# Performance work log

Hardware: AMD Instinct MI355X
Metric: run time of the kernel (lower is better)

Reference implementation:

```python
import jax, jax.numpy as jnp
import numpy as np

N_NODES = 100000
N_EDGES = 1600000
NFEAT, NHID1, NCLASS = 256, 128, 64
NUM_GRAPHS = 64


def gcn_conv(x, edge_index, edge_weight, W, b):
    # PyG GCNConv: linear transform, add self-loops (weight 1), symmetric norm, scatter-add
    n = x.shape[0]
    x = x @ W  # [N, out]
    loop = jnp.arange(n)
    row = jnp.concatenate([edge_index[0], loop])  # source
    col = jnp.concatenate([edge_index[1], loop])  # target
    w = jnp.concatenate([edge_weight, jnp.ones((n,), dtype=x.dtype)])
    deg = jax.ops.segment_sum(w, col, num_segments=n)
    dinv = jnp.where(deg > 0, jax.lax.rsqrt(jnp.maximum(deg, 1e-30)), 0.0)
    norm = dinv[row] * w * dinv[col]  # [E+N]
    out = jax.ops.segment_sum(x[row] * norm[:, None], col, num_segments=n)
    return out + b


def setup_inputs() -> dict:
    key = jax.random.key(0)
    ks = jax.random.split(key, 12)
    x = jax.random.normal(ks[0], (N_NODES, NFEAT), dtype=jnp.float32)
    edge_index = jax.random.randint(ks[1], (2, N_EDGES), 0, N_NODES, dtype=jnp.int64)
    edge_weight = jax.random.uniform(ks[2], (N_EDGES,), dtype=jnp.float32)
    batch = jnp.sort(jax.random.randint(ks[3], (N_NODES,), 0, NUM_GRAPHS, dtype=jnp.int64))
    def glorot(k, shape):
        lim = float(np.sqrt(6.0 / (shape[0] + shape[1])))
        return jax.random.uniform(k, shape, jnp.float32, -lim, lim)
    W1 = glorot(ks[4], (NFEAT, NHID1)); b1 = jnp.zeros((NHID1,), jnp.float32)
    W2 = glorot(ks[5], (NHID1, NCLASS)); b2 = jnp.zeros((NCLASS,), jnp.float32)
    l1w = glorot(ks[6], (NCLASS, 64)); l1b = jnp.zeros((64,), jnp.float32)
    l2w = glorot(ks[7], (64, 2)); l2b = jnp.zeros((2,), jnp.float32)
    return {"x": x, "edge_index": edge_index, "edge_weight": edge_weight, "batch": batch,
            "W1": W1, "b1": b1, "W2": W2, "b2": b2,
            "l1w": l1w, "l1b": l1b, "l2w": l2w, "l2b": l2b}


def reference(x, edge_index, edge_weight, batch, W1, b1, W2, b2, l1w, l1b, l2w, l2b):
    h = jax.nn.relu(gcn_conv(x, edge_index, edge_weight, W1, b1))
    h = jax.nn.relu(gcn_conv(h, edge_index, edge_weight, W2, b2))
    pooled = jax.ops.segment_sum(h, batch, num_segments=NUM_GRAPHS)  # global_add_pool
    h = jax.nn.relu(pooled @ l1w + l1b)
    out = h @ l2w + l2b
    Y_prob = jax.nn.log_softmax(out, axis=1)
    Y_hat = jnp.argmax(Y_prob, axis=1).astype(jnp.float32)
    return (Y_prob, Y_hat, out)
```

## Files before the change

kernel.cpp:

```cpp
#include <hip/hip_runtime.h>
#include <hip/hip_bf16.h>
#include <math.h>

#define N_NODES 100000
#define N_EDGES 1600000
#define NFEAT 256
#define NHID1 128
#define NCLASS 64
#define NUM_GRAPHS 64

#define POOL_CHUNK 64

#define NBUCK 391
#define EPB 8192
#define NBLK_A 196

typedef __attribute__((ext_vector_type(8))) short bf16x8;
typedef __attribute__((ext_vector_type(4))) float f32x4;


__device__ __forceinline__ unsigned short f2bf(float f) {
    unsigned u = __float_as_uint(f);
    u += 0x7fffu + ((u >> 16) & 1u);
    return (unsigned short)(u >> 16);
}
__device__ __forceinline__ unsigned packbf2(float lo, float hi) {
    return (unsigned)f2bf(lo) | ((unsigned)f2bf(hi) << 16);
}
__device__ __forceinline__ float bflo(unsigned p) { return __uint_as_float(p << 16); }
__device__ __forceinline__ float bfhi(unsigned p) { return __uint_as_float(p & 0xffff0000u); }


__global__ __launch_bounds__(256) void hist_kernel(const int* __restrict__ cols,
                                                   int* __restrict__ ghist, int nE) {
    __shared__ int h[NBUCK];
    const int tid = threadIdx.x;
    for (int i = tid; i < NBUCK; i += 256) h[i] = 0;
    __syncthreads();
    long base = (long)blockIdx.x * EPB;
    for (int j = tid; j < EPB; j += 256) {
        long idx = base + j;
        if (idx < nE) atomicAdd(&h[cols[idx] >> 8], 1);
    }
    __syncthreads();
    for (int i = tid; i < NBUCK; i += 256) {
        int v = h[i];
        if (v) atomicAdd(&ghist[i], v);
    }
}


__global__ __launch_bounds__(512) void bucket_scan_kernel(const int* __restrict__ ghist,
                                                          int* __restrict__ gbase,
                                                          int* __restrict__ gcursor) {
    __shared__ int sh[512];
    int t = threadIdx.x;
    int v = (t < NBUCK) ? ghist[t] : 0;
    sh[t] = v;
    __syncthreads();
    for (int off = 1; off < 512; off <<= 1) {
        int add = (t >= off) ? sh[t - off] : 0;
        __syncthreads();
        sh[t] += add;
        __syncthreads();
    }
    if (t < NBUCK) {
        int excl = sh[t] - v;
        gbase[t] = excl;
        gcursor[t] = excl;
    }
}


__global__ __launch_bounds__(256) void scatter_bucket_kernel(const int* __restrict__ rows,
                                                             const int* __restrict__ cols,
                                                             const float* __restrict__ w,
                                                             int* __restrict__ gcursor,
                                                             int2* __restrict__ csc_tmp, int nE) {
    __shared__ int h[NBUCK];
    __shared__ int bb[NBUCK];
    __shared__ unsigned short rk[EPB];
    const int tid = threadIdx.x;
    for (int i = tid; i < NBUCK; i += 256) h[i] = 0;
    __syncthreads();
    long base = (long)blockIdx.x * EPB;
    for (int j = tid; j < EPB; j += 256) {
        long idx = base + j;
        if (idx < nE) rk[j] = (unsigned short)atomicAdd(&h[cols[idx] >> 8], 1);
    }
    __syncthreads();
    for (int i = tid; i < NBUCK; i += 256) {
        int v = h[i];
        if (v) bb[i] = atomicAdd(&gcursor[i], v);
    }
    __syncthreads();
    for (int j = tid; j < EPB; j += 256) {
        long idx = base + j;
        if (idx < nE) {
            int c = cols[idx];
            int b = c >> 8;
            int pos = bb[b] + (int)rk[j];
            csc_tmp[pos] = make_int2((rows[idx] & 0x1FFFF) | ((c & 255) << 17),
                                     __float_as_int(w[idx]));
        }
    }
}


__global__ __launch_bounds__(256) void build_csc_kernel(const int2* __restrict__ csc_tmp,
                                                        const int* __restrict__ gbase,
                                                        const int* __restrict__ ghist,
                                                        int2* __restrict__ edges,
                                                        int* __restrict__ starts,
                                                        int* __restrict__ cnt,
                                                        float* __restrict__ dinv, int n) {
    __shared__ int ncnt[256];
    __shared__ float nws[256];
    __shared__ int sh[256];
    __shared__ int ncur[256];
    const int tid = threadIdx.x;
    const int b = blockIdx.x;
    const int base = gbase[b];
    const int cntb = ghist[b];

    ncnt[tid] = 0;
    nws[tid] = 0.f;
    __syncthreads();

    for (int i = tid; i < cntb; i += 256) {
        int2 rec = csc_tmp[base + i];
        int local = ((unsigned)rec.x) >> 17;
        atomicAdd(&ncnt[local], 1);
        atomicAdd(&nws[local], __int_as_float(rec.y));
    }
    __syncthreads();

    int v = ncnt[tid];
    sh[tid] = v;
    __syncthreads();
    for (int off = 1; off < 256; off <<= 1) {
        int add = (tid >= off) ? sh[tid - off] : 0;
        __syncthreads();
        sh[tid] += add;
        __syncthreads();
    }
    int excl = sh[tid] - v;
    ncur[tid] = excl;

    int node = (b << 8) + tid;
    if (node < n) {
        cnt[node] = v;
        starts[node] = base + excl;
        dinv[node] = rsqrtf(1.0f + nws[tid]);
    }
    __syncthreads();

    for (int i = tid; i < cntb; i += 256) {
        int2 rec = csc_tmp[base + i];
        int local = ((unsigned)rec.x) >> 17;
        int r = rec.x & 0x1FFFF;
        int pos = base + atomicAdd(&ncur[local], 1);
        edges[pos] = make_int2(r, rec.y);
    }
}


__global__ void transpose_bf_kernel(const float* __restrict__ W, unsigned* __restrict__ WT,
                                    int K, int Nn) {
    int idx = blockIdx.x * blockDim.x + threadIdx.x;
    int total = Nn * (K / 2);
    if (idx < total) {
        int n = idx / (K / 2);
        int kp = idx - n * (K / 2);
        WT[idx] = packbf2(W[(2 * kp) * Nn + n], W[(2 * kp + 1) * Nn + n]);
    }
}


template <int NT, int KK, bool ABF16>
__global__ __launch_bounds__(256) void gemm_mfma(const void* __restrict__ Av,
                                                 const unsigned* __restrict__ BT,
                                                 const float* __restrict__ rowscale,
                                                 unsigned short* __restrict__ C,
                                                 int M) {
    constexpr int CT = NT / 16;
    constexpr int KD = KK / 2;
    __shared__ unsigned Al[4][128][4];
    __shared__ unsigned Bl[4][NT][4];
    const int tid = threadIdx.x;
    const int wave = tid >> 6;
    const int lane = tid & 63;
    const int quad = lane >> 4;
    const int l16 = lane & 15;
    const int row0 = blockIdx.x * 128;

    f32x4 acc[2][CT] = {};

    for (int k0 = 0; k0 < KK; k0 += 32) {
        if (ABF16) {
            const unsigned* Ab = (const unsigned*)Av;
            #pragma unroll
            for (int i = 0; i < 2; i++) {
                int idx = tid + i * 256;
                int ar = idx >> 2, aq = idx & 3;
                uint4 v = make_uint4(0, 0, 0, 0);
                if (row0 + ar < M)
                    v = *(const uint4*)(Ab + (long)(row0 + ar) * KD + k0 / 2 + aq * 4);
                *(uint4*)&Al[aq][ar][0] = v;
            }
        } else {
            const float* Af = (const float*)Av;
            int ar = tid >> 1, ah = tid & 1;
            float4 v0 = make_float4(0, 0, 0, 0), v1 = v0, v2 = v0, v3 = v0;
            if (row0 + ar < M) {
                const float* p = Af + (long)(row0 + ar) * KK + k0 + ah * 16;
                v0 = *(const float4*)p;
                v1 = *(const float4*)(p + 4);
                v2 = *(const float4*)(p + 8);
                v3 = *(const float4*)(p + 12);
            }
            uint4 d0 = make_uint4(packbf2(v0.x, v0.y), packbf2(v0.z, v0.w),
                                  packbf2(v1.x, v1.y), packbf2(v1.z, v1.w));
            uint4 d1 = make_uint4(packbf2(v2.x, v2.y), packbf2(v2.z, v2.w),
                                  packbf2(v3.x, v3.y), packbf2(v3.z, v3.w));
            *(uint4*)&Al[ah * 2 + 0][ar][0] = d0;
            *(uint4*)&Al[ah * 2 + 1][ar][0] = d1;
        }
        #pragma unroll
        for (int i = 0; i < NT / 64; i++) {
            int idx = tid + i * 256;
            int br = idx >> 2, bq = idx & 3;
            *(uint4*)&Bl[bq][br][0] = *(const uint4*)(BT + (long)br * KD + k0 / 2 + bq * 4);
        }
        __syncthreads();

        bf16x8 af[2];
        #pragma unroll
        for (int rt = 0; rt < 2; rt++)
            af[rt] = *(const bf16x8*)&Al[quad][wave * 32 + rt * 16 + l16][0];
        #pragma unroll
        for (int ct = 0; ct < CT; ct++) {
            bf16x8 bfr = *(const bf16x8*)&Bl[quad][ct * 16 + l16][0];
            acc[0][ct] = __builtin_amdgcn_mfma_f32_16x16x32_bf16(af[0], bfr, acc[0][ct], 0, 0, 0);
            acc[1][ct] = __builtin_amdgcn_mfma_f32_16x16x32_bf16(af[1], bfr, acc[1][ct], 0, 0, 0);
        }
        __syncthreads();
    }

    #pragma unroll
    for (int rt = 0; rt < 2; rt++) {
        #pragma unroll
        for (int reg = 0; reg < 4; reg++) {
            int row = row0 + wave * 32 + rt * 16 + quad * 4 + reg;
            if (row < M) {
                float sc = rowscale[row];
                unsigned short* cp = C + (long)row * NT + l16;
                #pragma unroll
                for (int ct = 0; ct < CT; ct++)
                    cp[ct * 16] = f2bf(acc[rt][ct][reg] * sc);
            }
        }
    }
}


template <int F, bool RELU, bool BF16OUT>
__global__ __launch_bounds__(256) void gather_agg_bf(const unsigned* __restrict__ xsb,
                                                     const int2* __restrict__ edges,
                                                     const int* __restrict__ starts,
                                                     const int* __restrict__ cnt,
                                                     const float* __restrict__ dinv,
                                                     const float* __restrict__ bias,
                                                     void* __restrict__ outv, int n) {
    constexpr int G = F / 8;
    constexpr int FU = F / 2;
    int gt = blockIdx.x * blockDim.x + threadIdx.x;
    int node = gt / G;
    int lane = gt - node * G;
    if (node >= n) return;

    int s = starts[node];
    int c = cnt[node];
    int e = s + c;
    float acc[8] = {};
    const unsigned* lbase = xsb + lane * 4;

    int j = s;
    for (; j + 3 < e; j += 4) {
        int2 e0 = edges[j];
        int2 e1 = edges[j + 1];
        int2 e2 = edges[j + 2];
        int2 e3 = edges[j + 3];
        uint4 p0 = *(const uint4*)(lbase + (long)e0.x * FU);
        uint4 p1 = *(const uint4*)(lbase + (long)e1.x * FU);
        uint4 p2 = *(const uint4*)(lbase + (long)e2.x * FU);
        uint4 p3 = *(const uint4*)(lbase + (long)e3.x * FU);
        float w0 = __int_as_float(e0.y);
        float w1 = __int_as_float(e1.y);
        float w2 = __int_as_float(e2.y);
        float w3 = __int_as_float(e3.y);
        acc[0] += bflo(p0.x) * w0; acc[1] += bfhi(p0.x) * w0;
        acc[2] += bflo(p0.y) * w0; acc[3] += bfhi(p0.y) * w0;
        acc[4] += bflo(p0.z) * w0; acc[5] += bfhi(p0.z) * w0;
        acc[6] += bflo(p0.w) * w0; acc[7] += bfhi(p0.w) * w0;
        acc[0] += bflo(p1.x) * w1; acc[1] += bfhi(p1.x) * w1;
        acc[2] += bflo(p1.y) * w1; acc[3] += bfhi(p1.y) * w1;
        acc[4] += bflo(p1.z) * w1; acc[5] += bfhi(p1.z) * w1;
        acc[6] += bflo(p1.w) * w1; acc[7] += bfhi(p1.w) * w1;
        acc[0] += bflo(p2.x) * w2; acc[1] += bfhi(p2.x) * w2;
        acc[2] += bflo(p2.y) * w2; acc[3] += bfhi(p2.y) * w2;
        acc[4] += bflo(p2.z) * w2; acc[5] += bfhi(p2.z) * w2;
        acc[6] += bflo(p2.w) * w2; acc[7] += bfhi(p2.w) * w2;
        acc[0] += bflo(p3.x) * w3; acc[1] += bfhi(p3.x) * w3;
        acc[2] += bflo(p3.y) * w3; acc[3] += bfhi(p3.y) * w3;
        acc[4] += bflo(p3.z) * w3; acc[5] += bfhi(p3.z) * w3;
        acc[6] += bflo(p3.w) * w3; acc[7] += bfhi(p3.w) * w3;
    }
    for (; j < e; j++) {
        int2 ed = edges[j];
        float wv = __int_as_float(ed.y);
        uint4 p = *(const uint4*)(lbase + (long)ed.x * FU);
        acc[0] += bflo(p.x) * wv; acc[1] += bfhi(p.x) * wv;
        acc[2] += bflo(p.y) * wv; acc[3] += bfhi(p.y) * wv;
        acc[4] += bflo(p.z) * wv; acc[5] += bfhi(p.z) * wv;
        acc[6] += bflo(p.w) * wv; acc[7] += bfhi(p.w) * wv;
    }

    float d = dinv[node];
    uint4 sp = *(const uint4*)(lbase + (long)node * FU);
    float sv[8] = { bflo(sp.x), bfhi(sp.x), bflo(sp.y), bfhi(sp.y),
                    bflo(sp.z), bfhi(sp.z), bflo(sp.w), bfhi(sp.w) };
    float4 bb0 = ((const float4*)bias)[lane * 2];
    float4 bb1 = ((const float4*)bias)[lane * 2 + 1];
    float bbv[8] = { bb0.x, bb0.y, bb0.z, bb0.w, bb1.x, bb1.y, bb1.z, bb1.w };
    float r[8];
    #pragma unroll
    for (int i = 0; i < 8; i++) {
        float v = d * (acc[i] + sv[i]) + bbv[i];
        r[i] = RELU ? fmaxf(v, 0.f) : v;
    }
    if (BF16OUT) {
        unsigned* ob = (unsigned*)outv;
        uint4 pk = make_uint4(packbf2(r[0], r[1]), packbf2(r[2], r[3]),
                              packbf2(r[4], r[5]), packbf2(r[6], r[7]));
        *(uint4*)(ob + (long)node * FU + lane * 4) = pk;
    } else {
        float* o = (float*)outv + (long)node * F + lane * 8;
        *(float4*)o       = make_float4(r[0], r[1], r[2], r[3]);
        *(float4*)(o + 4) = make_float4(r[4], r[5], r[6], r[7]);
    }
}


__global__ void pool_kernel(const float* __restrict__ h,
                            const int* __restrict__ batch,
                            float* __restrict__ pooled,
                            int n) {
    int f = threadIdx.x;
    long start = (long)blockIdx.x * POOL_CHUNK;
    long end = start + POOL_CHUNK;
    if (end > n) end = n;
    if (start >= end) return;
    int cur = batch[start];
    float acc = 0.f;
    for (long i = start; i < end; i++) {
        int g = batch[i];
        if (g != cur) {
            atomicAdd(&pooled[cur * NCLASS + f], acc);
            acc = 0.f;
            cur = g;
        }
        acc += h[i * NCLASS + f];
    }
    atomicAdd(&pooled[cur * NCLASS + f], acc);
}


__global__ __launch_bounds__(256) void head_kernel(const float* __restrict__ pooled,
                                                   const float* __restrict__ l1w,
                                                   const float* __restrict__ l1b,
                                                   const float* __restrict__ l2w,
                                                   const float* __restrict__ l2b,
                                                   float* __restrict__ out) {
    __shared__ float P[64][68];
    __shared__ float W[64][68];
    __shared__ float red0[64][4];
    __shared__ float red1[64][4];
    const int tid = threadIdx.x;

    for (int i = tid; i < 1024; i += 256) {
        int r = i >> 4;
        int cq = (i & 15) * 4;
        *(float4*)&P[r][cq] = *(const float4*)&pooled[r * 64 + cq];
        *(float4*)&W[r][cq] = *(const float4*)&l1w[r * 64 + cq];
    }
    __syncthreads();

    const int g = tid >> 2;
    const int q = tid & 3;
    const int j0 = q * 16;

    float hacc[16];
    #pragma unroll
    for (int jj = 0; jj < 16; jj++) hacc[jj] = l1b[j0 + jj];

    for (int c = 0; c < 64; c++) {
        float pv = P[g][c];
        #pragma unroll
        for (int jj = 0; jj < 16; jj += 4) {
            float4 wv = *(const float4*)&W[c][j0 + jj];
            hacc[jj + 0] += pv * wv.x;
            hacc[jj + 1] += pv * wv.y;
            hacc[jj + 2] += pv * wv.z;
            hacc[jj + 3] += pv * wv.w;
        }
    }

    float o0 = 0.f, o1 = 0.f;
    #pragma unroll
    for (int jj = 0; jj < 16; jj++) {
        float h = fmaxf(hacc[jj], 0.f);
        o0 += h * l2w[(j0 + jj) * 2];
        o1 += h * l2w[(j0 + jj) * 2 + 1];
    }
    red0[g][q] = o0;
    red1[g][q] = o1;
    __syncthreads();

    if (q == 0) {
        float a0 = red0[g][0] + red0[g][1] + red0[g][2] + red0[g][3] + l2b[0];
        float a1 = red1[g][0] + red1[g][1] + red1[g][2] + red1[g][3] + l2b[1];
        float m = fmaxf(a0, a1);
        float lse = m + logf(expf(a0 - m) + expf(a1 - m));
        out[g * 2 + 0] = a0 - lse;
        out[g * 2 + 1] = a1 - lse;
        out[128 + g] = (a1 > a0) ? 1.f : 0.f;
        out[192 + g * 2 + 0] = a0;
        out[192 + g * 2 + 1] = a1;
    }
}


extern "C" void kernel_launch(void* const* d_in, const int* in_sizes, int n_in,
                              void* d_out, int out_size, void* d_ws, size_t ws_size,
                              hipStream_t stream) {
    const float* x   = (const float*)d_in[0];
    const int* eidx  = (const int*)d_in[1];
    const float* ew  = (const float*)d_in[2];
    const int* batch = (const int*)d_in[3];
    const float* W1  = (const float*)d_in[4];
    const float* b1  = (const float*)d_in[5];
    const float* W2  = (const float*)d_in[6];
    const float* b2  = (const float*)d_in[7];
    const float* l1w = (const float*)d_in[8];
    const float* l1b = (const float*)d_in[9];
    const float* l2w = (const float*)d_in[10];
    const float* l2b = (const float*)d_in[11];
    float* out = (float*)d_out;

    const int N = N_NODES, E = N_EDGES;
    const int* rows = eidx;
    const int* cols = eidx + E;

    float* ws = (float*)d_ws;
    int*   ghist   = (int*)ws;
    int*   gbase   = ghist + 512;
    int*   gcursor = gbase + 512;
    float* dinv    = (float*)(gcursor + 512);
    int*   cnt     = (int*)(dinv + N);
    int*   starts  = cnt + N;
    unsigned* w1t  = (unsigned*)(starts + N);
    unsigned* w2t  = w1t + 16384;
    int2*  csc_tmp = (int2*)(w2t + 4096);
    int2*  edges   = csc_tmp + E;
    unsigned* xsb  = (unsigned*)(edges + E);
    unsigned* h1b  = xsb + (long)N * 64;
    float* pooled  = (float*)(h1b + (long)N * 64);
    unsigned* hw2b = xsb;
    float* h2 = (float*)h1b;

    hipMemsetAsync(ghist, 0, 512 * sizeof(int), stream);
    hist_kernel<<<NBLK_A, 256, 0, stream>>>(cols, ghist, E);

    bucket_scan_kernel<<<1, 512, 0, stream>>>(ghist, gbase, gcursor);

    scatter_bucket_kernel<<<NBLK_A, 256, 0, stream>>>(rows, cols, ew, gcursor, csc_tmp, E);

    build_csc_kernel<<<NBUCK, 256, 0, stream>>>(csc_tmp, gbase, ghist, edges, starts, cnt, dinv, N);

    transpose_bf_kernel<<<64, 256, 0, stream>>>(W1, w1t, NFEAT, NHID1);
    transpose_bf_kernel<<<16, 256, 0, stream>>>(W2, w2t, NHID1, NCLASS);

    gemm_mfma<NHID1, NFEAT, false><<<(N + 127) / 128, 256, 0, stream>>>(
        x, w1t, dinv, (unsigned short*)xsb, N);

    {
        long threads = (long)N * (NHID1 / 8);
        gather_agg_bf<NHID1, true, true><<<(threads + 255) / 256, 256, 0, stream>>>(
            xsb, edges, starts, cnt, dinv, b1, h1b, N);
    }

    gemm_mfma<NCLASS, NHID1, true><<<(N + 127) / 128, 256, 0, stream>>>(
        h1b, w2t, dinv, (unsigned short*)hw2b, N);

    {
        long threads = (long)N * (NCLASS / 8);
        gather_agg_bf<NCLASS, true, false><<<(threads + 255) / 256, 256, 0, stream>>>(
            hw2b, edges, starts, cnt, dinv, b2, h2, N);
    }

    hipMemsetAsync(pooled, 0, NUM_GRAPHS * NCLASS * sizeof(float), stream);
    {
        int blocks = (N + POOL_CHUNK - 1) / POOL_CHUNK;
        pool_kernel<<<blocks, 64, 0, stream>>>(h2, batch, pooled, N);
    }

    head_kernel<<<1, 256, 0, stream>>>(pooled, l1w, l1b, l2w, l2b, out);
}
```

Before: 413.3 us.

## Fuse global add pool into second-layer aggregation and use nontemporal edge loads

The second GCN aggregation now reduces its ReLU outputs straight into per-graph sums. It accumulates in shared memory for up to four graphs relative to the block's first node and falls back to global atomics otherwise. This removes the fp32 h2 write and read and the separate pool kernel launch. Edge loads and the layer-1 bf16 output store now use nontemporal hints to reduce cache pollution. The cost is many shared-memory atomics per thread plus extra barriers, and nontemporal loads could hurt if the edge data was benefiting from cache.

```diff
diff --git a/kernel.cpp b/kernel.cpp
--- a/kernel.cpp
+++ b/kernel.cpp
@@ -9,14 +9,13 @@
 #define NCLASS 64
 #define NUM_GRAPHS 64
 
-#define POOL_CHUNK 64
-
 #define NBUCK 391
 #define EPB 8192
 #define NBLK_A 196
 
 typedef __attribute__((ext_vector_type(8))) short bf16x8;
 typedef __attribute__((ext_vector_type(4))) float f32x4;
+typedef __attribute__((ext_vector_type(4))) unsigned u32x4;
 
 
 __device__ __forceinline__ unsigned short f2bf(float f) {
@@ -264,115 +263,139 @@
 }
 
 
-template <int F, bool RELU, bool BF16OUT>
+template <int F, bool RELU, int OUTMODE>
 __global__ __launch_bounds__(256) void gather_agg_bf(const unsigned* __restrict__ xsb,
                                                      const int2* __restrict__ edges,
                                                      const int* __restrict__ starts,
                                                      const int* __restrict__ cnt,
                                                      const float* __restrict__ dinv,
                                                      const float* __restrict__ bias,
+                                                     const int* __restrict__ batch,
                                                      void* __restrict__ outv, int n) {
     constexpr int G = F / 8;
     constexpr int FU = F / 2;
     int gt = blockIdx.x * blockDim.x + threadIdx.x;
     int node = gt / G;
     int lane = gt - node * G;
-    if (node >= n) return;
-
-    int s = starts[node];
-    int c = cnt[node];
-    int e = s + c;
+
+    if (OUTMODE != 2 && node >= n) return;
+    bool active = (node < n);
+
+    __shared__ float lp[4][64];
+    int g0 = 0;
+    if (OUTMODE == 2) {
+        lp[threadIdx.x >> 6][threadIdx.x & 63] = 0.f;
+        int firstnode = (blockIdx.x * blockDim.x) / G;
+        if (firstnode >= n) firstnode = n - 1;
+        g0 = batch[firstnode];
+        __syncthreads();
+    }
+
     float acc[8] = {};
+    float d = 0.f;
     const unsigned* lbase = xsb + lane * 4;
 
-    int j = s;
-    for (; j + 3 < e; j += 4) {
-        int2 e0 = edges[j];
-        int2 e1 = edges[j + 1];
-        int2 e2 = edges[j + 2];
-        int2 e3 = edges[j + 3];
-        uint4 p0 = *(const uint4*)(lbase + (long)e0.x * FU);
-        uint4 p1 = *(const uint4*)(lbase + (long)e1.x * FU);
-        uint4 p2 = *(const uint4*)(lbase + (long)e2.x * FU);
-        uint4 p3 = *(const uint4*)(lbase + (long)e3.x * FU);
-        float w0 = __int_as_float(e0.y);
-        float w1 = __int_as_float(e1.y);
-        float w2 = __int_as_float(e2.y);
-        float w3 = __int_as_float(e3.y);
-        acc[0] += bflo(p0.x) * w0; acc[1] += bfhi(p0.x) * w0;
-        acc[2] += bflo(p0.y) * w0; acc[3] += bfhi(p0.y) * w0;
-        acc[4] += bflo(p0.z) * w0; acc[5] += bfhi(p0.z) * w0;
-        acc[6] += bflo(p0.w) * w0; acc[7] += bfhi(p0.w) * w0;
-        acc[0] += bflo(p1.x) * w1; acc[1] += bfhi(p1.x) * w1;
-        acc[2] += bflo(p1.y) * w1; acc[3] += bfhi(p1.y) * w1;
-        acc[4] += bflo(p1.z) * w1; acc[5] += bfhi(p1.z) * w1;
-        acc[6] += bflo(p1.w) * w1; acc[7] += bfhi(p1.w) * w1;
-        acc[0] += bflo(p2.x) * w2; acc[1] += bfhi(p2.x) * w2;
-        acc[2] += bflo(p2.y) * w2; acc[3] += bfhi(p2.y) * w2;
-        acc[4] += bflo(p2.z) * w2; acc[5] += bfhi(p2.z) * w2;
-        acc[6] += bflo(p2.w) * w2; acc[7] += bfhi(p2.w) * w2;
-        acc[0] += bflo(p3.x) * w3; acc[1] += bfhi(p3.x) * w3;
-        acc[2] += bflo(p3.y) * w3; acc[3] += bfhi(p3.y) * w3;
-        acc[4] += bflo(p3.z) * w3; acc[5] += bfhi(p3.z) * w3;
-        acc[6] += bflo(p3.w) * w3; acc[7] += bfhi(p3.w) * w3;
-    }
-    for (; j < e; j++) {
-        int2 ed = edges[j];
-        float wv = __int_as_float(ed.y);
-        uint4 p = *(const uint4*)(lbase + (long)ed.x * FU);
-        acc[0] += bflo(p.x) * wv; acc[1] += bfhi(p.x) * wv;
-        acc[2] += bflo(p.y) * wv; acc[3] += bfhi(p.y) * wv;
-        acc[4] += bflo(p.z) * wv; acc[5] += bfhi(p.z) * wv;
-        acc[6] += bflo(p.w) * wv; acc[7] += bfhi(p.w) * wv;
-    }
-
-    float d = dinv[node];
-    uint4 sp = *(const uint4*)(lbase + (long)node * FU);
-    float sv[8] = { bflo(sp.x), bfhi(sp.x), bflo(sp.y), bfhi(sp.y),
-                    bflo(sp.z), bfhi(sp.z), bflo(sp.w), bfhi(sp.w) };
-    float4 bb0 = ((const float4*)bias)[lane * 2];
-    float4 bb1 = ((const float4*)bias)[lane * 2 + 1];
-    float bbv[8] = { bb0.x, bb0.y, bb0.z, bb0.w, bb1.x, bb1.y, bb1.z, bb1.w };
-    float r[8];
-    #pragma unroll
-    for (int i = 0; i < 8; i++) {
-        float v = d * (acc[i] + sv[i]) + bbv[i];
-        r[i] = RELU ? fmaxf(v, 0.f) : v;
-    }
-    if (BF16OUT) {
-        unsigned* ob = (unsigned*)outv;
-        uint4 pk = make_uint4(packbf2(r[0], r[1]), packbf2(r[2], r[3]),
-                              packbf2(r[4], r[5]), packbf2(r[6], r[7]));
-        *(uint4*)(ob + (long)node * FU + lane * 4) = pk;
+    if (active) {
+        int s = starts[node];
+        int c = cnt[node];
+        int e = s + c;
+
+        int j = s;
+        for (; j + 3 < e; j += 4) {
+            long long q0 = __builtin_nontemporal_load((const long long*)(edges + j));
+            long long q1 = __builtin_nontemporal_load((const long long*)(edges + j + 1));
+            long long q2 = __builtin_nontemporal_load((const long long*)(edges + j + 2));
+            long long q3 = __builtin_nontemporal_load((const long long*)(edges + j + 3));
+            int r0 = (int)q0, r1 = (int)q1, r2 = (int)q2, r3 = (int)q3;
+            float w0 = __int_as_float((int)(q0 >> 32));
+            float w1 = __int_as_float((int)(q1 >> 32));
+            float w2 = __int_as_float((int)(q2 >> 32));
+            float w3 = __int_as_float((int)(q3 >> 32));
+            uint4 p0 = *(const uint4*)(lbase + (long)r0 * FU);
+            uint4 p1 = *(const uint4*)(lbase + (long)r1 * FU);
+            uint4 p2 = *(const uint4*)(lbase + (long)r2 * FU);
+            uint4 p3 = *(const uint4*)(lbase + (long)r3 * FU);
+            acc[0] += bflo(p0.x) * w0; acc[1] += bfhi(p0.x) * w0;
+            acc[2] += bflo(p0.y) * w0; acc[3] += bfhi(p0.y) * w0;
+            acc[4] += bflo(p0.z) * w0; acc[5] += bfhi(p0.z) * w0;
+            acc[6] += bflo(p0.w) * w0; acc[7] += bfhi(p0.w) * w0;
+            acc[0] += bflo(p1.x) * w1; acc[1] += bfhi(p1.x) * w1;
+            acc[2] += bflo(p1.y) * w1; acc[3] += bfhi(p1.y) * w1;
+            acc[4] += bflo(p1.z) * w1; acc[5] += bfhi(p1.z) * w1;
+            acc[6] += bflo(p1.w) * w1; acc[7] += bfhi(p1.w) * w1;
+            acc[0] += bflo(p2.x) * w2; acc[1] += bfhi(p2.x) * w2;
+            acc[2] += bflo(p2.y) * w2; acc[3] += bfhi(p2.y) * w2;
+            acc[4] += bflo(p2.z) * w2; acc[5] += bfhi(p2.z) * w2;
+            acc[6] += bflo(p2.w) * w2; acc[7] += bfhi(p2.w) * w2;
+            acc[0] += bflo(p3.x) * w3; acc[1] += bfhi(p3.x) * w3;
+            acc[2] += bflo(p3.y) * w3; acc[3] += bfhi(p3.y) * w3;
+            acc[4] += bflo(p3.z) * w3; acc[5] += bfhi(p3.z) * w3;
+            acc[6] += bflo(p3.w) * w3; acc[7] += bfhi(p3.w) * w3;
+        }
+        for (; j < e; j++) {
+            long long q = __builtin_nontemporal_load((const long long*)(edges + j));
+            int r = (int)q;
+            float wv = __int_as_float((int)(q >> 32));
+            uint4 p = *(const uint4*)(lbase + (long)r * FU);
+            acc[0] += bflo(p.x) * wv; acc[1] += bfhi(p.x) * wv;
+            acc[2] += bflo(p.y) * wv; acc[3] += bfhi(p.y) * wv;
+            acc[4] += bflo(p.z) * wv; acc[5] += bfhi(p.z) * wv;
+            acc[6] += bflo(p.w) * wv; acc[7] += bfhi(p.w) * wv;
+        }
+        d = dinv[node];
+    }
+
+    float r[8] = {};
+    if (active) {
+        uint4 sp = *(const uint4*)(lbase + (long)node * FU);
+        float sv[8] = { bflo(sp.x), bfhi(sp.x), bflo(sp.y), bfhi(sp.y),
+                        bflo(sp.z), bfhi(sp.z), bflo(sp.w), bfhi(sp.w) };
+        float4 bb0 = ((const float4*)bias)[lane * 2];
+        float4 bb1 = ((const float4*)bias)[lane * 2 + 1];
+        float bbv[8] = { bb0.x, bb0.y, bb0.z, bb0.w, bb1.x, bb1.y, bb1.z, bb1.w };
+        #pragma unroll
+        for (int i = 0; i < 8; i++) {
+            float v = d * (acc[i] + sv[i]) + bbv[i];
+            r[i] = RELU ? fmaxf(v, 0.f) : v;
+        }
+    }
+
+    if (OUTMODE == 1) {
+        if (active) {
+            unsigned* ob = (unsigned*)outv;
+            u32x4 pk = { packbf2(r[0], r[1]), packbf2(r[2], r[3]),
+                         packbf2(r[4], r[5]), packbf2(r[6], r[7]) };
+            __builtin_nontemporal_store(pk, (u32x4*)(ob + (long)node * FU + lane * 4));
+        }
+    } else if (OUTMODE == 0) {
+        if (active) {
+            float* o = (float*)outv + (long)node * F + lane * 8;
+            *(float4*)o       = make_float4(r[0], r[1], r[2], r[3]);
+            *(float4*)(o + 4) = make_float4(r[4], r[5], r[6], r[7]);
+        }
     } else {
-        float* o = (float*)outv + (long)node * F + lane * 8;
-        *(float4*)o       = make_float4(r[0], r[1], r[2], r[3]);
-        *(float4*)(o + 4) = make_float4(r[4], r[5], r[6], r[7]);
-    }
-}
-
-
-__global__ void pool_kernel(const float* __restrict__ h,
-                            const int* __restrict__ batch,
-                            float* __restrict__ pooled,
-                            int n) {
-    int f = threadIdx.x;
-    long start = (long)blockIdx.x * POOL_CHUNK;
-    long end = start + POOL_CHUNK;
-    if (end > n) end = n;
-    if (start >= end) return;
-    int cur = batch[start];
-    float acc = 0.f;
-    for (long i = start; i < end; i++) {
-        int g = batch[i];
-        if (g != cur) {
-            atomicAdd(&pooled[cur * NCLASS + f], acc);
-            acc = 0.f;
-            cur = g;
-        }
-        acc += h[i * NCLASS + f];
-    }
-    atomicAdd(&pooled[cur * NCLASS + f], acc);
+        float* pooled = (float*)outv;
+        if (active) {
+            int g = batch[node];
+            int rel = g - g0;
+            if (rel >= 0 && rel < 4) {
+                #pragma unroll
+                for (int i = 0; i < 8; i++)
+                    atomicAdd(&lp[rel][lane * 8 + i], r[i]);
+            } else {
+                #pragma unroll
+                for (int i = 0; i < 8; i++)
+                    atomicAdd(&pooled[g * 64 + lane * 8 + i], r[i]);
+            }
+        }
+        __syncthreads();
+        int idx = threadIdx.x;
+        int rel = idx >> 6, feat = idx & 63;
+        float v = lp[rel][feat];
+        int g = g0 + rel;
+        if (v != 0.f && g < NUM_GRAPHS)
+            atomicAdd(&pooled[g * 64 + feat], v);
+    }
 }
 
 
@@ -477,7 +500,6 @@
     unsigned* h1b  = xsb + (long)N * 64;
     float* pooled  = (float*)(h1b + (long)N * 64);
     unsigned* hw2b = xsb;
-    float* h2 = (float*)h1b;
 
     hipMemsetAsync(ghist, 0, 512 * sizeof(int), stream);
     hist_kernel<<<NBLK_A, 256, 0, stream>>>(cols, ghist, E);
@@ -496,23 +518,18 @@
 
     {
         long threads = (long)N * (NHID1 / 8);
-        gather_agg_bf<NHID1, true, true><<<(threads + 255) / 256, 256, 0, stream>>>(
-            xsb, edges, starts, cnt, dinv, b1, h1b, N);
+        gather_agg_bf<NHID1, true, 1><<<(threads + 255) / 256, 256, 0, stream>>>(
+            xsb, edges, starts, cnt, dinv, b1, batch, h1b, N);
     }
 
     gemm_mfma<NCLASS, NHID1, true><<<(N + 127) / 128, 256, 0, stream>>>(
         h1b, w2t, dinv, (unsigned short*)hw2b, N);
 
+    hipMemsetAsync(pooled, 0, NUM_GRAPHS * NCLASS * sizeof(float), stream);
     {
         long threads = (long)N * (NCLASS / 8);
-        gather_agg_bf<NCLASS, true, false><<<(threads + 255) / 256, 256, 0, stream>>>(
-            hw2b, edges, starts, cnt, dinv, b2, h2, N);
-    }
-
-    hipMemsetAsync(pooled, 0, NUM_GRAPHS * NCLASS * sizeof(float), stream);
-    {
-        int blocks = (N + POOL_CHUNK - 1) / POOL_CHUNK;
-        pool_kernel<<<blocks, 64, 0, stream>>>(h2, batch, pooled, N);
+        gather_agg_bf<NCLASS, true, 2><<<(threads + 255) / 256, 256, 0, stream>>>(
+            hw2b, edges, starts, cnt, dinv, b2, batch, pooled, N);
     }
 
     head_kernel<<<1, 256, 0, stream>>>(pooled, l1w, l1b, l2w, l2b, out);
```

After: 436.4 us. +5.6%, slower.
